# Optimization experiments

Hardware: AMD Instinct MI355X
Metric: run time of the kernel (lower is better)

## Reference

```python
import jax, jax.numpy as jnp
import numpy as np

# ---- static configuration (mirrors EarthSpecificBlock/EarthAttention3D) ----
WS = (2, 6, 12)                 # window_size (Z, H, W)
DIM = 192
HEADS = 6
DEPTH = 2
B, Z, H, W = 1, 8, 91, 180      # token grid entering the layer
PAD_H = (WS[1] - H % WS[1]) % WS[1]   # 5
PAD_W = (WS[2] - W % WS[2]) % WS[2]   # 0
HP, WP = H + PAD_H, W + PAD_W         # 96, 180
TOK = WS[0] * WS[1] * WS[2]           # 144 tokens per window
NZ, NH, NW = Z // WS[0], HP // WS[1], WP // WS[2]   # 4, 16, 15
TYPE_W = NZ * NH                      # 64 window types (Z x lat)
BIAS_ROWS = (2 * WS[2] - 1) * WS[1] * WS[1] * WS[0] * WS[0]  # 3312


def _construct_index():
    """Position index into the earth-specific bias table (EarthAttention3D._construct_index)."""
    zi = np.arange(WS[0]); zj = -np.arange(WS[0]) * WS[0]
    hi = np.arange(WS[1]); hj = -np.arange(WS[1]) * WS[1]
    w = np.arange(WS[2])
    c1 = np.stack(np.meshgrid(zi, hi, w, indexing='ij')).reshape(3, -1)
    c2 = np.stack(np.meshgrid(zj, hj, w, indexing='ij')).reshape(3, -1)
    coords = (c1[:, :, None] - c2[:, None, :]).transpose(1, 2, 0)
    coords[:, :, 2] += WS[2] - 1
    coords[:, :, 1] *= 2 * WS[2] - 1
    coords[:, :, 0] *= (2 * WS[2] - 1) * WS[1] * WS[1]
    return coords.sum(-1).reshape(-1)   # (TOK*TOK,)


def _gen_mask():
    """Shifted-window attention mask (gen_mask), shape (1, NW, TYPE_W, 1, TOK, TOK)."""
    m = np.zeros((1, Z, HP, WP, 1), np.float32)
    zs = (slice(0, -WS[0]), slice(-WS[0], -WS[0] // 2), slice(-WS[0] // 2, None))
    hs = (slice(0, -WS[1]), slice(-WS[1], -WS[1] // 2), slice(-WS[1] // 2, None))
    cnt = 0
    for zsl in zs:
        for hsl in hs:
            m[:, zsl, hsl, :, :] = cnt
            cnt += 1
    mw = m.reshape(1, NZ, WS[0], NH, WS[1], NW, WS[2], 1).transpose(0, 1, 3, 5, 2, 4, 6, 7)
    mw = mw.reshape(1, NZ, NH, NW, TOK)
    am = mw[:, :, :, :, None, :] - mw[:, :, :, :, :, None]
    am = np.where(am != 0, np.float32(-100.0), np.float32(0.0))
    return am.transpose(0, 3, 1, 2, 4, 5).reshape(1, NW, TYPE_W, 1, TOK, TOK)


POS_IDX = jnp.asarray(_construct_index())
MASK = jnp.asarray(_gen_mask())


def _ln(x, g, b):
    m = x.mean(-1, keepdims=True)
    v = ((x - m) ** 2).mean(-1, keepdims=True)
    return (x - m) * jax.lax.rsqrt(v + 1e-5) * g + b


def _block(x, qkv_w, qkv_b, proj_w, proj_b, bias_tab, g1, b1, g2, b2, w1, bm1, w2, bm2, roll):
    shortcut = x
    x = jnp.pad(x, ((0, 0), (0, 0), (0, PAD_H), (0, PAD_W), (0, 0)))
    if roll:
        x = jnp.roll(x, (-(WS[0] // 2), -(WS[1] // 2), -(WS[2] // 2)), axis=(1, 2, 3))
    # window partition: (B, NW, TYPE_W, TOK, C)
    xw = x.reshape(B, NZ, WS[0], NH, WS[1], NW, WS[2], DIM).transpose(0, 5, 1, 3, 2, 4, 6, 7)
    xw = xw.reshape(B, NW, TYPE_W, TOK, DIM)
    dh = DIM // HEADS
    qkv = (xw @ qkv_w + qkv_b).reshape(B, NW, TYPE_W, TOK, 3, HEADS, dh)
    qkv = qkv.transpose(4, 0, 1, 2, 5, 3, 6)   # (3, B, NW, TYPE_W, HEADS, TOK, dh)
    q, k, v = qkv[0], qkv[1], qkv[2]
    q = q * (dh ** -0.5)
    attn = jnp.einsum('bwphid,bwphjd->bwphij', q, k)
    bias = bias_tab[POS_IDX].reshape(TOK, TOK, TYPE_W, HEADS).transpose(2, 3, 0, 1)
    attn = attn + bias
    if roll:
        attn = attn + MASK
    attn = jax.nn.softmax(attn, axis=-1)
    out = jnp.einsum('bwphij,bwphjd->bwphid', attn, v)
    out = out.transpose(0, 1, 2, 4, 3, 5).reshape(B, NW, TYPE_W, TOK, DIM)
    out = out @ proj_w + proj_b
    # window merge back to (B, Z, HP, WP, C)
    x = out.reshape(B, NW, NZ, NH, WS[0], WS[1], WS[2], DIM).transpose(0, 2, 4, 3, 5, 1, 6, 7)
    x = x.reshape(B, Z, HP, WP, DIM)
    if roll:
        x = jnp.roll(x, (WS[0] // 2, WS[1] // 2, WS[2] // 2), axis=(1, 2, 3))
    x = x[:, :, :H, :W]
    x = shortcut + _ln(x, g1, b1)           # post-norm residual, as in source
    h = jax.nn.gelu(x @ w1 + bm1, approximate=False)
    h = h @ w2 + bm2
    return x + _ln(h, g2, b2)


def setup_inputs() -> dict:
    key = jax.random.key(0)
    ks = jax.random.split(key, 8)
    s = 0.02
    return {
        'x': jax.random.normal(ks[0], (B, Z, H, W, DIM), jnp.float32),
        'qkv_w': jax.random.normal(ks[1], (DEPTH, DIM, 3 * DIM), jnp.float32) * s,
        'qkv_b': jnp.zeros((DEPTH, 3 * DIM), jnp.float32),
        'proj_w': jax.random.normal(ks[2], (DEPTH, DIM, DIM), jnp.float32) * s,
        'proj_b': jnp.zeros((DEPTH, DIM), jnp.float32),
        'bias_tab': jax.random.normal(ks[3], (DEPTH, BIAS_ROWS, TYPE_W, HEADS), jnp.float32) * s,
        'norm1_g': jnp.ones((DEPTH, DIM), jnp.float32),
        'norm1_b': jnp.zeros((DEPTH, DIM), jnp.float32),
        'norm2_g': jnp.ones((DEPTH, DIM), jnp.float32),
        'norm2_b': jnp.zeros((DEPTH, DIM), jnp.float32),
        'mlp_w1': jax.random.normal(ks[4], (DEPTH, DIM, 4 * DIM), jnp.float32) * s,
        'mlp_b1': jnp.zeros((DEPTH, 4 * DIM), jnp.float32),
        'mlp_w2': jax.random.normal(ks[5], (DEPTH, 4 * DIM, DIM), jnp.float32) * s,
        'mlp_b2': jnp.zeros((DEPTH, DIM), jnp.float32),
    }


def reference(x, qkv_w, qkv_b, proj_w, proj_b, bias_tab, norm1_g, norm1_b,
              norm2_g, norm2_b, mlp_w1, mlp_b1, mlp_w2, mlp_b2):
    for i in range(DEPTH):
        x = _block(x, qkv_w[i], qkv_b[i], proj_w[i], proj_b[i], bias_tab[i],
                   norm1_g[i], norm1_b[i], norm2_g[i], norm2_b[i],
                   mlp_w1[i], mlp_b1[i], mlp_w2[i], mlp_b2[i], roll=(i % 2 == 1))
    return x
```

## Files before the change

kernel.cpp:

```cpp
#include <hip/hip_runtime.h>
#include <math.h>

#define NTOK   131040
#define NTOKW  138240

typedef __attribute__((ext_vector_type(8))) short bf16x8;
typedef __attribute__((ext_vector_type(8))) unsigned short u16x8;
typedef __attribute__((ext_vector_type(4))) float f32x4;
typedef __attribute__((ext_vector_type(2))) float f32x2;

__device__ __forceinline__ float b2f(unsigned short u){
  union { unsigned u; float f; } v; v.u = ((unsigned)u) << 16; return v.f;
}
__device__ __forceinline__ unsigned short f2b(float f){
  union { float f; unsigned u; } v; v.f = f;
  unsigned r = v.u + 0x7FFFu + ((v.u >> 16) & 1u);
  return (unsigned short)(r >> 16);
}
__device__ __forceinline__ float gelu_sig(float x){
  float e = __expf(-1.702f * x);
  return x * __builtin_amdgcn_rcpf(1.0f + e);
}
__device__ __forceinline__ unsigned pk_bf16(float lo, float hi){
  unsigned r;
  asm("v_cvt_pk_bf16_f32 %0, %1, %2" : "=v"(r) : "v"(lo), "v"(hi));
  return r;
}
__device__ __forceinline__ void lds_barrier(){
  asm volatile("s_waitcnt lgkmcnt(0)" ::: "memory");
  __builtin_amdgcn_sched_barrier(0);
  __builtin_amdgcn_s_barrier();
  __builtin_amdgcn_sched_barrier(0);
}

__global__ __launch_bounds__(256) void transp(const float* __restrict__ src,
                                              unsigned short* __restrict__ dst,
                                              int K, int N){
  int i = blockIdx.x*256 + threadIdx.x;
  if (i < K*N){
    int n = i / K, k = i % K;
    dst[i] = f2b(src[(size_t)k*N + n]);
  }
}

__global__ __launch_bounds__(256) void bias_pre(
    const float* __restrict__ btab,
    unsigned short* __restrict__ bw,
    int roll)
{
  int gid = blockIdx.x*256 + threadIdx.x;
  int pair = gid / 20736;
  int rem  = gid % 20736;
  int i = rem / 144, j = rem % 144;
  int tw = pair / 6, head = pair % 6;
  int ia = i/72, ib = (i%72)/12, ic = i%12;
  int ja = j/72, jb = (j%72)/12, jc = j%12;
  int idx = (ia + 2*ja)*828 + (ib + 6*jb)*23 + (ic - jc + 11);
  float v = btab[(size_t)idx*384 + tw*6 + head];
  if (roll){
    int nz = tw >> 4, nh = tw & 15;
    int zi = nz*2+ia, hi = nh*6+ib, zj = nz*2+ja, hj = nh*6+jb;
    int ri = 3*((zi<6)?0:((zi<7)?1:2)) + ((hi<90)?0:((hi<93)?1:2));
    int rj = 3*((zj<6)?0:((zj<7)?1:2)) + ((hj<90)?0:((hj<93)?1:2));
    if (ri != rj) v -= 100.0f;
  }
  bw[gid] = f2b(v);
}

__global__ __launch_bounds__(256) void gather_win(const float* __restrict__ x,
                                                  unsigned short* __restrict__ xw,
                                                  int roll){
  int gid = blockIdx.x*256 + threadIdx.x;
  int row = gid / 24;
  int dp  = gid % 24;
  int tok = row % 144;
  int wt  = row / 144;
  int tw  = wt & 63;
  int w   = wt >> 6;
  int nz = tw >> 4, nh = tw & 15;
  int wz = tok / 72; int rem = tok % 72; int wh = rem / 12; int ww = rem % 12;
  int z = nz*2 + wz, h = nh*6 + wh, wc = w*12 + ww;
  if (roll){ z = (z+1)&7; h = (h+3)%96; wc = (wc+6)%180; }
  int d0 = dp*8;
  u16x8 o;
  if (h < 91){
    const float* s = x + ((size_t)((z*91 + h)*180 + wc))*192 + d0;
    #pragma unroll
    for (int i=0;i<8;i++) o[i] = f2b(s[i]);
  } else {
    #pragma unroll
    for (int i=0;i<8;i++) o[i] = 0;
  }
  *(u16x8*)(xw + (size_t)row*192 + d0) = o;
}

__global__ __launch_bounds__(512) void gemm_k192(
    const unsigned short* __restrict__ A,
    const unsigned short* __restrict__ Bt,
    const float* __restrict__ bias,
    unsigned short* __restrict__ C,
    int N)
{
  __shared__ unsigned short Bst[192][200];
  int m0 = blockIdx.x * 128;
  int n0 = blockIdx.y * 192;
  int t = threadIdx.x;
  int lane = t & 63, w = t >> 6;
  int wm = w >> 2, wn = w & 3;
  int lg = lane >> 4, lr = lane & 15;

  #pragma unroll
  for (int i=0;i<9;i++){
    int idx = t + i*512;
    int r = idx / 24, c = (idx % 24)*8;
    *(u16x8*)&Bst[r][c] = *(const u16x8*)(Bt + (size_t)(n0 + r)*192 + c);
  }
  __syncthreads();

  const unsigned short* aRow = A + (size_t)(m0 + wm*64 + lr)*192 + lg*8;

  f32x4 acc[4][3];
  #pragma unroll
  for (int a=0;a<4;a++)
    #pragma unroll
    for (int b=0;b<3;b++) acc[a][b] = (f32x4){0.f,0.f,0.f,0.f};

  bf16x8 aP[2][6];
  #pragma unroll
  for (int ks=0; ks<6; ks++) aP[0][ks] = *(const bf16x8*)(aRow + ks*32);

  #pragma unroll
  for (int rt=0; rt<4; rt++){
    if (rt < 3){
      const unsigned short* an = aRow + (size_t)(rt+1)*16*192;
      #pragma unroll
      for (int ks=0; ks<6; ks++) aP[(rt+1)&1][ks] = *(const bf16x8*)(an + ks*32);
    }
    #pragma unroll
    for (int ks=0; ks<6; ks++){
      bf16x8 b0 = *(const bf16x8*)&Bst[wn*48 +      lr][ks*32 + lg*8];
      bf16x8 b1 = *(const bf16x8*)&Bst[wn*48 + 16 + lr][ks*32 + lg*8];
      bf16x8 b2 = *(const bf16x8*)&Bst[wn*48 + 32 + lr][ks*32 + lg*8];
      bf16x8 af = aP[rt&1][ks];
      acc[rt][0] = __builtin_amdgcn_mfma_f32_16x16x32_bf16(af, b0, acc[rt][0], 0,0,0);
      acc[rt][1] = __builtin_amdgcn_mfma_f32_16x16x32_bf16(af, b1, acc[rt][1], 0,0,0);
      acc[rt][2] = __builtin_amdgcn_mfma_f32_16x16x32_bf16(af, b2, acc[rt][2], 0,0,0);
    }
  }

  #pragma unroll
  for (int rt=0; rt<4; rt++){
    #pragma unroll
    for (int fn=0; fn<3; fn++){
      int colg = n0 + wn*48 + fn*16 + lr;
      float bv = bias[colg];
      #pragma unroll
      for (int r=0;r<4;r++){
        int rowg = m0 + wm*64 + rt*16 + lg*4 + r;
        C[(size_t)rowg*N + colg] = f2b(acc[rt][fn][r] + bv);
      }
    }
  }
}

__global__ __launch_bounds__(576) void attn_win(
    const unsigned short* __restrict__ qkv,
    const unsigned short* __restrict__ bw,
    unsigned short* __restrict__ outp)
{
  __shared__ union {
    struct { unsigned short Qs[144][32]; unsigned short Ks[144][40]; } qk;
    unsigned short Ps[144][160];
  } U;
  __shared__ unsigned short Vst[32][160];

  int b = blockIdx.x;
  int head = b % 6;
  int wt = b / 6;
  int tw = wt & 63;
  int t = threadIdx.x;
  int lane = t & 63;
  int wv = t >> 6;
  int lg = lane >> 4, lr = lane & 15;

  {
    int tok = t >> 2, c0 = (t & 3)*8;
    size_t base = ((size_t)wt*144 + tok)*576 + head*32 + c0;
    u16x8 qv = *(const u16x8*)(qkv + base);
    u16x8 kv = *(const u16x8*)(qkv + base + 192);
    u16x8 vv = *(const u16x8*)(qkv + base + 384);
    u16x8 qs;
    #pragma unroll
    for (int i=0;i<8;i++) qs[i] = f2b(b2f(qv[i]) * 0.17677669529663687f);
    *(u16x8*)&U.qk.Qs[tok][c0] = qs;
    *(u16x8*)&U.qk.Ks[tok][c0] = kv;
    #pragma unroll
    for (int i=0;i<8;i++) Vst[c0+i][tok] = vv[i];
  }
  if (t < 512) Vst[t >> 4][144 + (t & 15)] = 0;
  __syncthreads();

  float s[9][4];
  {
    bf16x8 a = *(const bf16x8*)&U.qk.Qs[wv*16 + lr][lg*8];
    #pragma unroll
    for (int ct=0; ct<9; ct++){
      bf16x8 bb = *(const bf16x8*)&U.qk.Ks[ct*16 + lr][lg*8];
      f32x4 d = {0.f,0.f,0.f,0.f};
      d = __builtin_amdgcn_mfma_f32_16x16x32_bf16(a, bb, d, 0,0,0);
      s[ct][0]=d[0]; s[ct][1]=d[1]; s[ct][2]=d[2]; s[ct][3]=d[3];
    }
  }

  {
    const unsigned short* bp = bw + (size_t)(tw*6 + head)*20736;
    int i0 = wv*16 + lg*4;
    #pragma unroll
    for (int ct=0; ct<9; ct++){
      int j = ct*16 + lr;
      #pragma unroll
      for (int r=0;r<4;r++)
        s[ct][r] += b2f(bp[(i0 + r)*144 + j]);
    }
  }

  float mx[4] = {-1e30f,-1e30f,-1e30f,-1e30f};
  #pragma unroll
  for (int ct=0; ct<9; ct++)
    #pragma unroll
    for (int r=0;r<4;r++) mx[r] = fmaxf(mx[r], s[ct][r]);
  #pragma unroll
  for (int off=1; off<16; off<<=1)
    #pragma unroll
    for (int r=0;r<4;r++) mx[r] = fmaxf(mx[r], __shfl_xor(mx[r], off));
  float sm[4] = {0.f,0.f,0.f,0.f};
  #pragma unroll
  for (int ct=0; ct<9; ct++)
    #pragma unroll
    for (int r=0;r<4;r++){ s[ct][r] = __expf(s[ct][r] - mx[r]); sm[r] += s[ct][r]; }
  #pragma unroll
  for (int off=1; off<16; off<<=1)
    #pragma unroll
    for (int r=0;r<4;r++) sm[r] += __shfl_xor(sm[r], off);
  float inv[4];
  #pragma unroll
  for (int r=0;r<4;r++) inv[r] = 1.0f / sm[r];

  lds_barrier();

  #pragma unroll
  for (int ct=0; ct<9; ct++)
    #pragma unroll
    for (int r=0;r<4;r++)
      U.Ps[wv*16 + lg*4 + r][ct*16 + lr] = f2b(s[ct][r] * inv[r]);
  #pragma unroll
  for (int r=0;r<4;r++) U.Ps[wv*16 + lg*4 + r][144 + lr] = 0;
  __syncthreads();

  #pragma unroll
  for (int ct2=0; ct2<2; ct2++){
    f32x4 o = {0.f,0.f,0.f,0.f};
    #pragma unroll
    for (int kt=0; kt<5; kt++){
      bf16x8 a  = *(const bf16x8*)&U.Ps[wv*16 + lr][kt*32 + lg*8];
      bf16x8 bb = *(const bf16x8*)&Vst[ct2*16 + lr][kt*32 + lg*8];
      o = __builtin_amdgcn_mfma_f32_16x16x32_bf16(a, bb, o, 0,0,0);
    }
    size_t rb = ((size_t)wt*144 + wv*16 + lg*4)*192 + head*32 + ct2*16 + lr;
    #pragma unroll
    for (int r=0;r<4;r++) outp[rb + (size_t)r*192] = f2b(o[r]);
  }
}

__global__ __launch_bounds__(256) void unwin_ln(
  const unsigned short* __restrict__ ywin,
  const float* __restrict__ xsrc,
  const float* __restrict__ g, const float* __restrict__ bb,
  float* __restrict__ outf, unsigned short* __restrict__ outb, int roll)
{
  int tok = blockIdx.x*4 + (threadIdx.x>>6);
  if (tok >= NTOK) return;
  int lane = threadIdx.x & 63;
  int z = tok / (91*180);
  int rem = tok % (91*180);
  int h = rem / 180, wc = rem % 180;
  int zz=z, hh=h, ww=wc;
  if (roll){ zz = (z+7)&7; hh = (h+93)%96; ww = (wc+174)%180; }
  int nz = zz>>1, wz = zz&1;
  int nh = hh/6,  wh = hh%6;
  int nw = ww/12, w2 = ww%12;
  size_t row = ((size_t)(nw*64 + nz*16 + nh))*144 + wz*72 + wh*12 + w2;
  const unsigned short* yr = ywin + row*192;
  float v[3]; float s=0.f, ss=0.f;
  #pragma unroll
  for (int i=0;i<3;i++){ v[i] = b2f(yr[lane + i*64]); s += v[i]; ss += v[i]*v[i]; }
  #pragma unroll
  for (int off=32; off>=1; off>>=1){ s += __shfl_xor(s, off); ss += __shfl_xor(ss, off); }
  float mean = s * (1.0f/192.0f);
  float var = ss * (1.0f/192.0f) - mean*mean;
  float rinv = rsqrtf(var + 1e-5f);
  size_t tb = (size_t)tok*192;
  #pragma unroll
  for (int i=0;i<3;i++){
    int d = lane + i*64;
    float o = xsrc[tb + d] + ((v[i]-mean)*rinv*g[d] + bb[d]);
    outf[tb+d] = o;
    outb[tb+d] = f2b(o);
  }
}

__global__ __launch_bounds__(512) void mlp_fused_ln(
    const unsigned short* __restrict__ A,
    const unsigned short* __restrict__ W1t,
    const float* __restrict__ bias1,
    const unsigned short* __restrict__ W2t,
    const float* __restrict__ mbias2,
    const float* __restrict__ xmid,
    const float* __restrict__ lng,
    const float* __restrict__ lnb,
    float* __restrict__ outF,
    int M)
{
  __shared__ unsigned short W1s[32][196];
  __shared__ unsigned short W2s[192][44];
  __shared__ unsigned short Hs[8][16][40];
  __shared__ float b1s[768];
  __shared__ float eps[576];
  int m0 = blockIdx.x*128;
  int t = threadIdx.x, lane = t & 63, w = t >> 6;
  int lg = lane >> 4, lr = lane & 15;

  int arow = m0 + w*16 + lr;
  bf16x8 afr[6];
  if (arow < M){
    const unsigned short* ap = A + (size_t)arow*192 + lg*8;
    #pragma unroll
    for (int ks=0; ks<6; ks++) afr[ks] = *(const bf16x8*)(ap + ks*32);
  } else {
    #pragma unroll
    for (int ks=0; ks<6; ks++)
      #pragma unroll
      for (int j=0;j<8;j++) afr[ks][j] = 0;
  }

  b1s[t] = bias1[t];
  if (t < 256) b1s[512 + t] = bias1[512 + t];
  if (t < 192){ eps[t] = mbias2[t]; eps[192 + t] = lng[t]; eps[384 + t] = lnb[t]; }

  int i1r[2], i1c[2], i2r[2], i2c[2];
  #pragma unroll
  for (int i=0;i<2;i++){
    int idx = t + i*512;
    i1r[i] = idx/24; i1c[i] = (idx%24)*8;
    i2r[i] = idx/4;  i2c[i] = (idx&3)*8;
  }
  bool g2nd = (t + 512) < 768;

  u16x8 w1r[2], w2r[2];
  w1r[0] = *(const u16x8*)(W1t + (size_t)i1r[0]*192 + i1c[0]);
  w2r[0] = *(const u16x8*)(W2t + (size_t)i2r[0]*768 + i2c[0]);
  if (g2nd){
    w1r[1] = *(const u16x8*)(W1t + (size_t)i1r[1]*192 + i1c[1]);
    w2r[1] = *(const u16x8*)(W2t + (size_t)i2r[1]*768 + i2c[1]);
  }

  f32x4 acc[12];
  #pragma unroll
  for (int i=0;i<12;i++) acc[i] = (f32x4){0.f,0.f,0.f,0.f};

  for (int it=0; it<24; ++it){
    int hc = it*32;
    *(u16x8*)&W1s[i1r[0]][i1c[0]] = w1r[0];
    *(u16x8*)&W2s[i2r[0]][i2c[0]] = w2r[0];
    if (g2nd){
      *(u16x8*)&W1s[i1r[1]][i1c[1]] = w1r[1];
      *(u16x8*)&W2s[i2r[1]][i2c[1]] = w2r[1];
    }
    if (it < 23){
      int hc2 = hc + 32;
      w1r[0] = *(const u16x8*)(W1t + (size_t)(hc2 + i1r[0])*192 + i1c[0]);
      w2r[0] = *(const u16x8*)(W2t + (size_t)i2r[0]*768 + hc2 + i2c[0]);
      if (g2nd){
        w1r[1] = *(const u16x8*)(W1t + (size_t)(hc2 + i1r[1])*192 + i1c[1]);
        w2r[1] = *(const u16x8*)(W2t + (size_t)i2r[1]*768 + hc2 + i2c[1]);
      }
    }
    lds_barrier();

    f32x4 h0 = (f32x4){0.f,0.f,0.f,0.f};
    f32x4 h1 = (f32x4){0.f,0.f,0.f,0.f};
    #pragma unroll
    for (int ks=0; ks<6; ks++){
      bf16x8 b0  = *(const bf16x8*)&W1s[2*lr    ][ks*32 + lg*8];
      bf16x8 b1f = *(const bf16x8*)&W1s[2*lr + 1][ks*32 + lg*8];
      h0 = __builtin_amdgcn_mfma_f32_16x16x32_bf16(afr[ks], b0, h0, 0,0,0);
      h1 = __builtin_amdgcn_mfma_f32_16x16x32_bf16(afr[ks], b1f, h1, 0,0,0);
    }
    float bb0 = b1s[hc + 2*lr];
    float bb1 = b1s[hc + 2*lr + 1];
    #pragma unroll
    for (int r=0;r<4;r++){
      unsigned pk = pk_bf16(gelu_sig(h0[r] + bb0), gelu_sig(h1[r] + bb1));
      *(unsigned*)&Hs[w][lg*4 + r][2*lr] = pk;
    }
    bf16x8 pa = *(const bf16x8*)&Hs[w][lr][lg*8];
    #pragma unroll
    for (int f=0; f<6; f++){
      bf16x8 c0 = *(const bf16x8*)&W2s[f*32 + 2*lr    ][lg*8];
      bf16x8 c1 = *(const bf16x8*)&W2s[f*32 + 2*lr + 1][lg*8];
      acc[2*f]   = __builtin_amdgcn_mfma_f32_16x16x32_bf16(pa, c0, acc[2*f],   0,0,0);
      acc[2*f+1] = __builtin_amdgcn_mfma_f32_16x16x32_bf16(pa, c1, acc[2*f+1], 0,0,0);
    }
    lds_barrier();
  }

  #pragma unroll
  for (int r=0;r<4;r++){
    int row = m0 + w*16 + lg*4 + r;
    float s = 0.f, ss = 0.f;
    #pragma unroll
    for (int f=0; f<6; f++){
      float v0 = acc[2*f][r]   + eps[f*32 + 2*lr];
      float v1 = acc[2*f+1][r] + eps[f*32 + 2*lr + 1];
      s += v0 + v1; ss += v0*v0 + v1*v1;
    }
    #pragma unroll
    for (int off=1; off<16; off<<=1){ s += __shfl_xor(s, off); ss += __shfl_xor(ss, off); }
    float mean = s * (1.0f/192.0f);
    float var  = ss * (1.0f/192.0f) - mean*mean;
    float rinv = rsqrtf(var + 1e-5f);
    if (row < M){
      size_t base = (size_t)row*192;
      #pragma unroll
      for (int f=0; f<6; f++){
        int c0 = f*32 + 2*lr;
        float v0 = acc[2*f][r]   + eps[c0];
        float v1 = acc[2*f+1][r] + eps[c0 + 1];
        f32x2 xm = *(const f32x2*)&xmid[base + c0];
        f32x2 o;
        o[0] = xm[0] + (v0 - mean)*rinv*eps[192 + c0]     + eps[384 + c0];
        o[1] = xm[1] + (v1 - mean)*rinv*eps[192 + c0 + 1] + eps[384 + c0 + 1];
        *(f32x2*)&outF[base + c0] = o;
      }
    }
  }
}

extern "C" void kernel_launch(void* const* d_in, const int* in_sizes, int n_in,
                              void* d_out, int out_size, void* d_ws, size_t ws_size,
                              hipStream_t stream)
{
  const float* x_in    = (const float*)d_in[0];
  const float* qkvw    = (const float*)d_in[1];
  const float* qkvbias = (const float*)d_in[2];
  const float* projw   = (const float*)d_in[3];
  const float* projbias= (const float*)d_in[4];
  const float* btab    = (const float*)d_in[5];
  const float* n1g = (const float*)d_in[6];
  const float* n1b = (const float*)d_in[7];
  const float* n2g = (const float*)d_in[8];
  const float* n2b = (const float*)d_in[9];
  const float* w1  = (const float*)d_in[10];
  const float* b1  = (const float*)d_in[11];
  const float* w2  = (const float*)d_in[12];
  const float* b2  = (const float*)d_in[13];
  float* outp = (float*)d_out;

  const size_t REG_A = (size_t)NTOKW*192;
  const size_t REG_B = (size_t)NTOKW*576;
  const size_t W_QT  = (size_t)2*576*192;
  const size_t W_PT  = (size_t)2*192*192;
  const size_t W_1T  = (size_t)2*768*192;
  const size_t W_2T  = (size_t)2*192*768;
  const size_t TOT_SH = REG_A + REG_B + W_QT + W_PT + W_1T + W_2T;
  const size_t NEEDED = TOT_SH*2 + (size_t)NTOK*192*4;
  if (ws_size < NEEDED) return;

  unsigned short* ws16 = (unsigned short*)d_ws;
  size_t off = 0;
  unsigned short* regA = ws16 + off; off += REG_A;
  unsigned short* regB = ws16 + off; off += REG_B;
  unsigned short* wqt  = ws16 + off; off += W_QT;
  unsigned short* wpt  = ws16 + off; off += W_PT;
  unsigned short* w1t  = ws16 + off; off += W_1T;
  unsigned short* w2t  = ws16 + off; off += W_2T;
  float* xmidf = (float*)(ws16 + off);
  unsigned short* bw = (unsigned short*)xmidf;

  for (int dep=0; dep<2; dep++){
    transp<<<(192*576+255)/256,256,0,stream>>>(qkvw + (size_t)dep*192*576,
                                               wqt + (size_t)dep*576*192, 192, 576);
    transp<<<(192*192+255)/256,256,0,stream>>>(projw + (size_t)dep*192*192,
                                               wpt + (size_t)dep*192*192, 192, 192);
    transp<<<(192*768+255)/256,256,0,stream>>>(w1 + (size_t)dep*192*768,
                                               w1t + (size_t)dep*768*192, 192, 768);
    transp<<<(768*192+255)/256,256,0,stream>>>(w2 + (size_t)dep*768*192,
                                               w2t + (size_t)dep*192*768, 768, 192);
  }

  for (int dep=0; dep<2; dep++){
    int roll = dep;
    const float* xs = (dep==0) ? x_in : outp;
    float* xout = outp;

    gather_win<<<NTOKW*24/256, 256, 0, stream>>>(xs, regA, roll);

    dim3 g1(NTOKW/128, 3);
    gemm_k192<<<g1, 512, 0, stream>>>(regA, wqt + (size_t)dep*576*192,
                                      qkvbias + dep*576, regB, 576);

    bias_pre<<<(64*6*20736)/256, 256, 0, stream>>>(btab + (size_t)dep*3312*384, bw, roll);

    attn_win<<<960*6, 576, 0, stream>>>(regB, bw, regA);

    dim3 g2(NTOKW/128, 1);
    gemm_k192<<<g2, 512, 0, stream>>>(regA, wpt + (size_t)dep*192*192,
                                      projbias + dep*192, regB, 192);

    unwin_ln<<<NTOK/4, 256, 0, stream>>>(regB, xs, n1g + dep*192, n1b + dep*192,
                                         xmidf, regA, roll);

    mlp_fused_ln<<<(NTOK+127)/128, 512, 0, stream>>>(
        regA, w1t + (size_t)dep*768*192, b1 + dep*768,
        w2t + (size_t)dep*192*768, b2 + dep*192,
        xmidf, n2g + dep*192, n2b + dep*192, xout, NTOK);
  }
}
```

Before: 1.155 ms.

## Double rows per wave in fused MLP kernel and switch to tanh-form GELU

Each wave in the fused MLP+LayerNorm kernel now processes two 16-row tiles instead of one, so every W1/W2 fragment read from LDS feeds twice as many MFMAs. The block covers 256 rows, which halves the grid and the number of times each block stages the weights. The cost is roughly double the accumulator and A-fragment registers per thread, which may lower occupancy with fewer blocks in flight. The GELU is also changed from the sigmoid approximation to the tanh formula, which likely matches the reference more closely but costs a few extra ALU ops per element.

```diff
diff --git a/kernel.cpp b/kernel.cpp
--- a/kernel.cpp
+++ b/kernel.cpp
@@ -17,9 +17,11 @@
   unsigned r = v.u + 0x7FFFu + ((v.u >> 16) & 1u);
   return (unsigned short)(r >> 16);
 }
-__device__ __forceinline__ float gelu_sig(float x){
-  float e = __expf(-1.702f * x);
-  return x * __builtin_amdgcn_rcpf(1.0f + e);
+__device__ __forceinline__ float gelu_fast(float x){
+  float t = 0.79788456080286536f * (x + 0.044715f * x * x * x);
+  float e = __expf(2.0f * t);
+  float th = 1.0f - 2.0f * __builtin_amdgcn_rcpf(e + 1.0f);
+  return 0.5f * x * (1.0f + th);
 }
 __device__ __forceinline__ unsigned pk_bf16(float lo, float hi){
   unsigned r;
@@ -323,24 +325,36 @@
 {
   __shared__ unsigned short W1s[32][196];
   __shared__ unsigned short W2s[192][44];
-  __shared__ unsigned short Hs[8][16][40];
+  __shared__ unsigned short Hs[8][32][40];
   __shared__ float b1s[768];
   __shared__ float eps[576];
-  int m0 = blockIdx.x*128;
+  int m0 = blockIdx.x*256;
   int t = threadIdx.x, lane = t & 63, w = t >> 6;
   int lg = lane >> 4, lr = lane & 15;
 
-  int arow = m0 + w*16 + lr;
-  bf16x8 afr[6];
-  if (arow < M){
-    const unsigned short* ap = A + (size_t)arow*192 + lg*8;
-    #pragma unroll
-    for (int ks=0; ks<6; ks++) afr[ks] = *(const bf16x8*)(ap + ks*32);
-  } else {
-    #pragma unroll
-    for (int ks=0; ks<6; ks++)
-      #pragma unroll
-      for (int j=0;j<8;j++) afr[ks][j] = 0;
+  bf16x8 afrA[6], afrB[6];
+  {
+    int ra = m0 + w*32 + lr, rb = ra + 16;
+    if (ra < M){
+      const unsigned short* ap = A + (size_t)ra*192 + lg*8;
+      #pragma unroll
+      for (int ks=0; ks<6; ks++) afrA[ks] = *(const bf16x8*)(ap + ks*32);
+    } else {
+      #pragma unroll
+      for (int ks=0; ks<6; ks++)
+        #pragma unroll
+        for (int j=0;j<8;j++) afrA[ks][j] = 0;
+    }
+    if (rb < M){
+      const unsigned short* ap = A + (size_t)rb*192 + lg*8;
+      #pragma unroll
+      for (int ks=0; ks<6; ks++) afrB[ks] = *(const bf16x8*)(ap + ks*32);
+    } else {
+      #pragma unroll
+      for (int ks=0; ks<6; ks++)
+        #pragma unroll
+        for (int j=0;j<8;j++) afrB[ks][j] = 0;
+    }
   }
 
   b1s[t] = bias1[t];
@@ -364,9 +378,9 @@
     w2r[1] = *(const u16x8*)(W2t + (size_t)i2r[1]*768 + i2c[1]);
   }
 
-  f32x4 acc[12];
-  #pragma unroll
-  for (int i=0;i<12;i++) acc[i] = (f32x4){0.f,0.f,0.f,0.f};
+  f32x4 accA[12], accB[12];
+  #pragma unroll
+  for (int i=0;i<12;i++){ accA[i] = (f32x4){0.f,0.f,0.f,0.f}; accB[i] = (f32x4){0.f,0.f,0.f,0.f}; }
 
   for (int it=0; it<24; ++it){
     int hc = it*32;
@@ -387,60 +401,70 @@
     }
     lds_barrier();
 
-    f32x4 h0 = (f32x4){0.f,0.f,0.f,0.f};
-    f32x4 h1 = (f32x4){0.f,0.f,0.f,0.f};
+    f32x4 h0a = (f32x4){0.f,0.f,0.f,0.f}, h1a = h0a, h0b = h0a, h1b = h0a;
     #pragma unroll
     for (int ks=0; ks<6; ks++){
       bf16x8 b0  = *(const bf16x8*)&W1s[2*lr    ][ks*32 + lg*8];
       bf16x8 b1f = *(const bf16x8*)&W1s[2*lr + 1][ks*32 + lg*8];
-      h0 = __builtin_amdgcn_mfma_f32_16x16x32_bf16(afr[ks], b0, h0, 0,0,0);
-      h1 = __builtin_amdgcn_mfma_f32_16x16x32_bf16(afr[ks], b1f, h1, 0,0,0);
+      h0a = __builtin_amdgcn_mfma_f32_16x16x32_bf16(afrA[ks], b0,  h0a, 0,0,0);
+      h1a = __builtin_amdgcn_mfma_f32_16x16x32_bf16(afrA[ks], b1f, h1a, 0,0,0);
+      h0b = __builtin_amdgcn_mfma_f32_16x16x32_bf16(afrB[ks], b0,  h0b, 0,0,0);
+      h1b = __builtin_amdgcn_mfma_f32_16x16x32_bf16(afrB[ks], b1f, h1b, 0,0,0);
     }
     float bb0 = b1s[hc + 2*lr];
     float bb1 = b1s[hc + 2*lr + 1];
     #pragma unroll
     for (int r=0;r<4;r++){
-      unsigned pk = pk_bf16(gelu_sig(h0[r] + bb0), gelu_sig(h1[r] + bb1));
-      *(unsigned*)&Hs[w][lg*4 + r][2*lr] = pk;
-    }
-    bf16x8 pa = *(const bf16x8*)&Hs[w][lr][lg*8];
+      *(unsigned*)&Hs[w][lg*4 + r][2*lr] =
+          pk_bf16(gelu_fast(h0a[r] + bb0), gelu_fast(h1a[r] + bb1));
+      *(unsigned*)&Hs[w][16 + lg*4 + r][2*lr] =
+          pk_bf16(gelu_fast(h0b[r] + bb0), gelu_fast(h1b[r] + bb1));
+    }
+    bf16x8 paA = *(const bf16x8*)&Hs[w][lr][lg*8];
+    bf16x8 paB = *(const bf16x8*)&Hs[w][16 + lr][lg*8];
     #pragma unroll
     for (int f=0; f<6; f++){
       bf16x8 c0 = *(const bf16x8*)&W2s[f*32 + 2*lr    ][lg*8];
       bf16x8 c1 = *(const bf16x8*)&W2s[f*32 + 2*lr + 1][lg*8];
-      acc[2*f]   = __builtin_amdgcn_mfma_f32_16x16x32_bf16(pa, c0, acc[2*f],   0,0,0);
-      acc[2*f+1] = __builtin_amdgcn_mfma_f32_16x16x32_bf16(pa, c1, acc[2*f+1], 0,0,0);
+      accA[2*f]   = __builtin_amdgcn_mfma_f32_16x16x32_bf16(paA, c0, accA[2*f],   0,0,0);
+      accA[2*f+1] = __builtin_amdgcn_mfma_f32_16x16x32_bf16(paA, c1, accA[2*f+1], 0,0,0);
+      accB[2*f]   = __builtin_amdgcn_mfma_f32_16x16x32_bf16(paB, c0, accB[2*f],   0,0,0);
+      accB[2*f+1] = __builtin_amdgcn_mfma_f32_16x16x32_bf16(paB, c1, accB[2*f+1], 0,0,0);
     }
     lds_barrier();
   }
 
   #pragma unroll
-  for (int r=0;r<4;r++){
-    int row = m0 + w*16 + lg*4 + r;
-    float s = 0.f, ss = 0.f;
-    #pragma unroll
-    for (int f=0; f<6; f++){
-      float v0 = acc[2*f][r]   + eps[f*32 + 2*lr];
-      float v1 = acc[2*f+1][r] + eps[f*32 + 2*lr + 1];
-      s += v0 + v1; ss += v0*v0 + v1*v1;
-    }
-    #pragma unroll
-    for (int off=1; off<16; off<<=1){ s += __shfl_xor(s, off); ss += __shfl_xor(ss, off); }
-    float mean = s * (1.0f/192.0f);
-    float var  = ss * (1.0f/192.0f) - mean*mean;
-    float rinv = rsqrtf(var + 1e-5f);
-    if (row < M){
-      size_t base = (size_t)row*192;
+  for (int gsel=0; gsel<2; gsel++){
+    f32x4* acc = gsel ? accB : accA;
+    #pragma unroll
+    for (int r=0;r<4;r++){
+      int row = m0 + w*32 + gsel*16 + lg*4 + r;
+      float s = 0.f, ss = 0.f;
       #pragma unroll
       for (int f=0; f<6; f++){
-        int c0 = f*32 + 2*lr;
-        float v0 = acc[2*f][r]   + eps[c0];
-        float v1 = acc[2*f+1][r] + eps[c0 + 1];
-        f32x2 xm = *(const f32x2*)&xmid[base + c0];
-        f32x2 o;
-        o[0] = xm[0] + (v0 - mean)*rinv*eps[192 + c0]     + eps[384 + c0];
-        o[1] = xm[1] + (v1 - mean)*rinv*eps[192 + c0 + 1] + eps[384 + c0 + 1];
-        *(f32x2*)&outF[base + c0] = o;
+        float v0 = acc[2*f][r]   + eps[f*32 + 2*lr];
+        float v1 = acc[2*f+1][r] + eps[f*32 + 2*lr + 1];
+        s += v0 + v1; ss += v0*v0 + v1*v1;
+      }
+      #pragma unroll
+      for (int off=1; off<16; off<<=1){ s += __shfl_xor(s, off); ss += __shfl_xor(ss, off); }
+      float mean = s * (1.0f/192.0f);
+      float var  = ss * (1.0f/192.0f) - mean*mean;
+      float rinv = rsqrtf(var + 1e-5f);
+      if (row < M){
+        size_t base = (size_t)row*192;
+        #pragma unroll
+        for (int f=0; f<6; f++){
+          int c0 = f*32 + 2*lr;
+          float v0 = acc[2*f][r]   + eps[c0];
+          float v1 = acc[2*f+1][r] + eps[c0 + 1];
+          f32x2 xm = *(const f32x2*)&xmid[base + c0];
+          f32x2 o;
+          o[0] = xm[0] + (v0 - mean)*rinv*eps[192 + c0]     + eps[384 + c0];
+          o[1] = xm[1] + (v1 - mean)*rinv*eps[192 + c0 + 1] + eps[384 + c0 + 1];
+          *(f32x2*)&outF[base + c0] = o;
+        }
       }
     }
   }
@@ -520,7 +544,7 @@
     unwin_ln<<<NTOK/4, 256, 0, stream>>>(regB, xs, n1g + dep*192, n1b + dep*192,
                                          xmidf, regA, roll);
 
-    mlp_fused_ln<<<(NTOK+127)/128, 512, 0, stream>>>(
+    mlp_fused_ln<<<(NTOK+255)/256, 512, 0, stream>>>(
         regA, w1t + (size_t)dep*768*192, b1 + dep*768,
         w2t + (size_t)dep*192*768, b2 + dep*192,
         xmidf, n2g + dep*192, n2b + dep*192, xout, NTOK);
```

Result: faster. 1.083 ms (-6.2%).
